# Optimization experiments

Measured on AMD Instinct MI355X. Metric: run time of the kernel, lower is better.

## Reference

```python
import jax, jax.numpy as jnp
import numpy as np

N_NODES = 100000
N_USER = 50000
D_IN = 100     # n_units[0]
F_OUT = 16     # n_units[1]
N_HEAD = 3     # n_heads[0]
N_TYPES = 3    # nb_nodes
N_EDGES = 1600000
D2 = 128


def setup_inputs() -> dict:
    key = jax.random.key(0)
    ks = jax.random.split(key, 9)
    h = jax.random.normal(ks[0], (N_NODES, D_IN), dtype=jnp.float32)
    edge_index = jax.random.randint(ks[1], (N_TYPES, 2, N_EDGES), 0, N_NODES, dtype=jnp.int64)
    # per-type GAT params (torch Linear stored transposed: (in, out))
    W = jax.random.normal(ks[2], (N_TYPES, D_IN, N_HEAD * F_OUT), dtype=jnp.float32) * 0.1
    b = jax.random.normal(ks[3], (N_TYPES, N_HEAD * F_OUT), dtype=jnp.float32) * 0.1
    a_src = jax.random.normal(ks[4], (N_TYPES, N_HEAD, F_OUT), dtype=jnp.float32) * 0.1
    a_trg = jax.random.normal(ks[5], (N_TYPES, N_HEAD, F_OUT), dtype=jnp.float32) * 0.1
    # additive attention params
    w1 = jax.random.normal(ks[6], (D_IN, D2), dtype=jnp.float32) * 0.1
    w2 = jax.random.normal(ks[7], (F_OUT, D2), dtype=jnp.float32) * 0.1
    m = jax.random.normal(ks[8], (D2, 1), dtype=jnp.float32) * 0.1
    return {"h": h, "W": W, "b": b, "a_src": a_src, "a_trg": a_trg,
            "w1": w1, "w2": w2, "m": m, "edge_index": edge_index}


def _sparse_gat(h, src, trg, W, b, a_src, a_trg):
    """Single SparseMultiHeadGraphAttention layer followed by head-mean."""
    N = h.shape[0]
    h_prime = (h @ W + b).reshape(N, N_HEAD, F_OUT)  # (N, H, F)
    hs = h_prime[src]                                # (E', H, F) edge gather
    # NOTE: faithful to source — both scores use the src-gathered features
    e = (hs * a_src).sum(-1) + (hs * a_trg).sum(-1)  # (E', H)
    e = jax.nn.leaky_relu(e, negative_slope=0.2)
    e = e - e.max()                                  # global max (as in source)
    exp_e = jnp.exp(e)
    denom = jax.ops.segment_sum(exp_e, trg, num_segments=N)      # (N, H)
    alpha = exp_e / (denom[trg] + 1e-10)                          # (E', H)
    out = jax.ops.segment_sum(hs * alpha[..., None], trg, num_segments=N)  # (N, H, F)
    return out.mean(axis=1)  # == permute(1,0,2).mean(dim=0)


def reference(h, W, b, a_src, a_trg, w1, w2, m, edge_index):
    N = h.shape[0]
    loop = jnp.arange(N, dtype=edge_index.dtype)
    embs = []
    for t in range(N_TYPES):  # small fixed set of relation types
        src = jnp.concatenate([edge_index[t, 0], loop])  # add self-loops
        trg = jnp.concatenate([edge_index[t, 1], loop])
        x = _sparse_gat(h, src, trg, W[t], b[t], a_src[t], a_trg[t])
        embs.append(x[:N_USER])
    type_aware = jnp.stack(embs, axis=1)  # (Nu, |Rs|, F)
    feat = h[:N_USER]                     # (Nu, D)
    # additive attention over types
    q = jnp.tanh((feat @ w1)[:, None, :] + type_aware @ w2)  # (Nu, |Rs|, D2)
    scores = (q @ m)[..., 0]                                  # (Nu, |Rs|)
    beta = jax.nn.softmax(scores, axis=1)
    fusion = jnp.einsum('nr,nrf->nf', beta, type_aware)[:, None, :]  # (Nu,1,F)
    return jnp.concatenate([fusion, type_aware], axis=1)  # (Nu, |Rs|+1, F)
```

## Files before the change

kernel.cpp:

```cpp
#include <hip/hip_runtime.h>
#include <hip/hip_bf16.h>

#define N_NODES 100000
#define N_USER  50000
#define D_IN    100
#define F_OUT   16
#define N_HEAD  3
#define N_TYPES 3
#define N_EDGES 1600000
#define D2      128
#define N_SEG   (N_TYPES * N_USER)
#define KP      136
#define CAP     64
#define CAPH    32
#define NBLK    ((N_NODES + 63) / 64)
#define NPAIR   (N_TYPES * N_EDGES / 2)
#define NBIN    256
#define SEGB    586
#define NBLKA   782
#define PAIRS_A 3072
#define CAPPB   40

typedef __hip_bfloat16 bf16;
typedef __attribute__((ext_vector_type(8))) short bf16x8;
typedef __attribute__((ext_vector_type(4))) float f32x4;
static __device__ __forceinline__ float b2f(bf16 x) { return __bfloat162float(x); }

#define OFF_CVT   64
#define OFF_CW    (OFF_CVT)
#define OFF_CB    (OFF_CW + 14400)
#define OFF_CAS   (OFF_CB + 144)
#define OFF_CAT   (OFF_CAS + 144)
#define OFF_CW1   (OFF_CAT + 144)
#define OFF_CW2   (OFF_CW1 + 12800)
#define OFF_CM    (OFF_CW2 + 2048)
#define CVT_TOTAL 29808
#define OFF_WT    29888
#define OFF_REC   49472
#define OFF_BUCKET OFF_REC
#define OFF_CPB   (OFF_REC + 9600000)
#define OFF_CA    (OFF_CPB + 240000)
#define OFF_CB2   (OFF_CA + 151000)
#define OFF_ELIST (OFF_CB2 + 151000)
#define OFF_TA    (OFF_ELIST + 9600000)
#define OFF_FW1   (OFF_TA + 2400000)

__global__ void k_detect(const unsigned* __restrict__ hraw,
                         const unsigned* __restrict__ eiraw,
                         int* __restrict__ flags) {
    __shared__ int sane, nz;
    if (threadIdx.x == 0) { sane = 0; nz = 0; }
    __syncthreads();
    int cnt = 0; unsigned o = 0;
    for (int i = threadIdx.x; i < 1024; i += 256) {
        unsigned w = hraw[i];
        unsigned e = (w >> 23) & 0xFF;
        if (e >= 64 && e <= 200) cnt++;
        o |= eiraw[2 * i + 1];
    }
    atomicAdd(&sane, cnt);
    atomicOr(&nz, (int)(o != 0));
    __syncthreads();
    if (threadIdx.x == 0) {
        flags[0] = (sane > 512) ? 1 : 0;
        flags[1] = nz ? 0 : 1;
    }
}

#define NBLK_CVT 117
#define NBLK_WT  153
__global__ __launch_bounds__(256) void k_prep(
        const void* __restrict__ W, const void* __restrict__ b,
        const void* __restrict__ as_, const void* __restrict__ at_,
        const void* __restrict__ w1, const void* __restrict__ w2,
        const void* __restrict__ m, const int* __restrict__ flags,
        float* __restrict__ cvt, ushort* __restrict__ wt) {
    if (blockIdx.x < NBLK_CVT) {
        int i = blockIdx.x * 256 + threadIdx.x;
        if (i >= CVT_TOTAL) return;
        const void* src; int off;
        if      (i < 14400)                 { src = W;   off = i; }
        else if (i < 14400+144)             { src = b;   off = i - 14400; }
        else if (i < 14400+288)             { src = as_; off = i - 14544; }
        else if (i < 14400+432)             { src = at_; off = i - 14688; }
        else if (i < 14400+432+12800)       { src = w1;  off = i - 14832; }
        else if (i < 14400+432+12800+2048)  { src = w2;  off = i - 27632; }
        else                                { src = m;   off = i - 29680; }
        cvt[i] = flags[0] ? ((const float*)src)[off] : b2f(((const bf16*)src)[off]);
    } else {
        int i = (blockIdx.x - NBLK_CVT) * 256 + threadIdx.x;
        if (i >= 6 * 48 * KP) return;
        int g = i / (48 * KP);
        int r = i - g * (48 * KP);
        int n = r / KP, k = r % KP;
        ushort v = 0;
        if (k < D_IN) {
            if (g < 3) {
                size_t src = ((size_t)g * D_IN + k) * 48 + n;
                if (flags[0]) { bf16 x = __float2bfloat16(((const float*)W)[src]); v = *(ushort*)&x; }
                else          { v = ((const ushort*)W)[src]; }
            } else {
                int c = (g - 3) * 48 + n;
                if (c < D2) {
                    size_t src = (size_t)k * D2 + c;
                    if (flags[0]) { bf16 x = __float2bfloat16(((const float*)w1)[src]); v = *(ushort*)&x; }
                    else          { v = ((const ushort*)w1)[src]; }
                }
            }
        }
        wt[i] = v;
    }
}

static __device__ __forceinline__ int2 load_ei2(const void* ei, int f64, size_t pairPos) {
    if (f64) {
        int4 v = ((const int4*)ei)[pairPos];
        int2 r; r.x = v.x; r.y = v.z; return r;
    }
    return ((const int2*)ei)[pairPos];
}

__global__ __launch_bounds__(256) void k_part(const void* __restrict__ ei,
                                              const int* __restrict__ flags,
                                              unsigned* __restrict__ bucket,
                                              unsigned* __restrict__ cpb) {
    __shared__ int bc[NBIN];
    const int f64ei = flags[1];
    const int NE2 = N_EDGES >> 1;
    const int tid = threadIdx.x;
    const int blk = blockIdx.x;
    if (tid < NBIN) bc[tid] = 0;
    __syncthreads();
    const int pair0 = blk * PAIRS_A;
    int npair = NPAIR - pair0; if (npair > PAIRS_A) npair = PAIRS_A;
#pragma unroll
    for (int q = 0; q < PAIRS_A / 256; ++q) {
        int pp = q * 256 + tid;
        int ok = (pp < npair);
        int pg = pair0 + (ok ? pp : 0);
        int t  = (pg >= 2 * NE2) ? 2 : ((pg >= NE2) ? 1 : 0);
        int ep = pg - t * NE2;
        int2 tg = load_ei2(ei, f64ei, (size_t)(t * 2 + 1) * NE2 + ep);
        int2 sr = load_ei2(ei, f64ei, (size_t)(t * 2) * NE2 + ep);
        if (ok && (unsigned)tg.x < N_USER) {
            int seg = t * N_USER + tg.x;
            int bin = seg & 255;
            int pos = atomicAdd(&bc[bin], 1);
            if (pos < CAPPB)
                bucket[((size_t)bin * NBLKA + blk) * CAPPB + pos] =
                    ((unsigned)(seg >> 8) << 17) | (unsigned)sr.x;
        }
        if (ok && (unsigned)tg.y < N_USER) {
            int seg = t * N_USER + tg.y;
            int bin = seg & 255;
            int pos = atomicAdd(&bc[bin], 1);
            if (pos < CAPPB)
                bucket[((size_t)bin * NBLKA + blk) * CAPPB + pos] =
                    ((unsigned)(seg >> 8) << 17) | (unsigned)sr.y;
        }
    }
    __syncthreads();
    if (tid < NBIN) cpb[(size_t)tid * NBLKA + blk] = (unsigned)bc[tid];
}

__global__ __launch_bounds__(256) void k_place(const unsigned* __restrict__ bucket,
                                               const unsigned* __restrict__ cpb,
                                               int* __restrict__ elist,
                                               unsigned* __restrict__ cA,
                                               unsigned* __restrict__ cBv) {
    __shared__ int sc[SEGB];
    const int bin = blockIdx.x >> 1;
    const int h   = blockIdx.x & 1;
    const int tid = threadIdx.x;
    for (int i = tid; i < SEGB; i += 256) sc[i] = 0;
    __syncthreads();
    const int rn = NBLKA / 2;
    for (int j = tid; j < rn; j += 256) {
        int r = 2 * j + h;
        int c = (int)cpb[(size_t)bin * NBLKA + r];
        if (c > CAPPB) c = CAPPB;
        size_t base = ((size_t)bin * NBLKA + r) * CAPPB;
        for (int i4 = 0; i4 < (c + 3) >> 2; ++i4) {
            uint4 wv = *(const uint4*)&bucket[base + 4 * i4];
#pragma unroll
            for (int k = 0; k < 4; ++k) {
                int idx = 4 * i4 + k;
                if (idx < c) {
                    unsigned e = (k == 0) ? wv.x : (k == 1) ? wv.y : (k == 2) ? wv.z : wv.w;
                    int sl  = (int)(e >> 17);
                    int src = (int)(e & 0x1FFFFu);
                    int pos = atomicAdd(&sc[sl], 1);
                    if (pos < CAPH) {
                        int seg = (sl << 8) + bin;
                        int t = seg / N_USER;
                        elist[(size_t)seg * CAP + (h << 5) + pos] =
                            (t * N_NODES + src) << 7;
                    }
                }
            }
        }
    }
    __syncthreads();
    for (int s = tid; s < SEGB; s += 256) {
        int seg = (s << 8) + bin;
        if (seg < N_SEG) {
            int cc = sc[s]; if (cc > CAPH) cc = CAPH;
            if (h) cBv[seg] = (unsigned)cc; else cA[seg] = (unsigned)cc;
        }
    }
}

__global__ __launch_bounds__(256) void k_hp_pack(const void* __restrict__ h,
                                                 const ushort* __restrict__ wtg,
                                                 const float* __restrict__ cb,
                                                 const float* __restrict__ cas,
                                                 const float* __restrict__ cat,
                                                 const int* __restrict__ flags,
                                                 float* __restrict__ fw1G,
                                                 float* __restrict__ rec) {
    __shared__ alignas(16) ushort hs[64][KP];
    __shared__ alignas(16) unsigned img[64 * 36];
    const int tid = threadIdx.x;
    const int node0 = blockIdx.x * 64;
    const int f32in = flags[0];
    for (int i = tid; i < 64 * KP; i += 256) {
        int r = i / KP, c = i % KP;
        int n = node0 + r;
        ushort v = 0;
        if (c < D_IN && n < N_NODES) {
            if (f32in) {
                bf16 t16 = __float2bfloat16(((const float*)h)[(size_t)n * D_IN + c]);
                v = *(ushort*)&t16;
            } else {
                v = ((const ushort*)h)[(size_t)n * D_IN + c];
            }
        }
        hs[r][c] = v;
    }
    __syncthreads();
    const int lane = tid & 63;
    const int w    = tid >> 6;
    const int m    = lane & 15;
    const int quad = lane >> 4;
    ushort* img16 = (ushort*)img;
    const int elig = (node0 < N_USER);
    const int nphase = elig ? 6 : 3;
    for (int p = 0; p < nphase; ++p) {
        const ushort* wp = wtg + (size_t)p * 48 * KP;
        f32x4 acc0 = {0.f, 0.f, 0.f, 0.f}, acc1 = acc0, acc2 = acc0;
#pragma unroll
        for (int ks = 0; ks < 4; ++ks) {
            int ko = ks * 32 + quad * 8;
            bf16x8 a  = *(const bf16x8*)&hs[w * 16 + m][ko];
            bf16x8 b0 = *(const bf16x8*)&wp[(0 * 16 + m) * KP + ko];
            bf16x8 b1 = *(const bf16x8*)&wp[(1 * 16 + m) * KP + ko];
            bf16x8 b2 = *(const bf16x8*)&wp[(2 * 16 + m) * KP + ko];
            acc0 = __builtin_amdgcn_mfma_f32_16x16x32_bf16(a, b0, acc0, 0, 0, 0);
            acc1 = __builtin_amdgcn_mfma_f32_16x16x32_bf16(a, b1, acc1, 0, 0, 0);
            acc2 = __builtin_amdgcn_mfma_f32_16x16x32_bf16(a, b2, acc2, 0, 0, 0);
        }
        if (p < 3) {
            const int t = p;
            float hpv[3][4], sred[3][4];
#pragma unroll
            for (int nt = 0; nt < 3; ++nt) {
                int col = nt * 16 + m;
                float bv = cb[t * 48 + col];
                float av = cas[t * 48 + col] + cat[t * 48 + col];
                f32x4 a4 = (nt == 0) ? acc0 : (nt == 1) ? acc1 : acc2;
#pragma unroll
                for (int r = 0; r < 4; ++r) {
                    hpv[nt][r] = a4[r] + bv;
                    sred[nt][r] = hpv[nt][r] * av;
                }
            }
#pragma unroll
            for (int d = 1; d < 16; d <<= 1) {
#pragma unroll
                for (int nt = 0; nt < 3; ++nt)
#pragma unroll
                    for (int r = 0; r < 4; ++r)
                        sred[nt][r] += __shfl_xor(sred[nt][r], d);
            }
            float pk[3][4];
#pragma unroll
            for (int nt = 0; nt < 3; ++nt)
#pragma unroll
                for (int r = 0; r < 4; ++r) {
                    float s = sred[nt][r];
                    s = (s > 0.f) ? s : 0.2f * s;
                    pk[nt][r] = __expf(s);
                }
            __syncthreads();
#pragma unroll
            for (int nt = 0; nt < 3; ++nt) {
                int col = nt * 16 + m;
#pragma unroll
                for (int r = 0; r < 4; ++r) {
                    int row = w * 16 + quad * 4 + r;
                    bf16 gb = __float2bfloat16(pk[nt][r] * hpv[nt][r]);
                    img16[row * 72 + col] = *(ushort*)&gb;
                }
            }
            if (m < 8) {
#pragma unroll
                for (int r = 0; r < 4; ++r) {
                    int row = w * 16 + quad * 4 + r;
                    img[row * 36 + 24 + m] = (m < 3) ? __float_as_uint(pk[m][r]) : 0u;
                }
            }
            __syncthreads();
            {
                int r = tid >> 2, q = tid & 3;
                int n = node0 + r;
                if (n < N_NODES) {
                    const uint4* s = (const uint4*)&img[r * 36 + q * 8];
                    uint4 x0 = s[0], x1 = s[1];
                    uint4* d = (uint4*)((unsigned*)rec + ((size_t)t * N_NODES + n) * 32 + q * 8);
                    d[0] = x0; d[1] = x1;
                }
            }
        } else {
            const int chunk = p - 3;
#pragma unroll
            for (int nt = 0; nt < 3; ++nt) {
                int col = chunk * 48 + nt * 16 + m;
                if (col < D2) {
                    f32x4 a4 = (nt == 0) ? acc0 : (nt == 1) ? acc1 : acc2;
#pragma unroll
                    for (int r = 0; r < 4; ++r) {
                        int row = w * 16 + quad * 4 + r;
                        int v = node0 + row;
                        if (v < N_USER) fw1G[(size_t)v * D2 + col] = a4[r];
                    }
                }
            }
        }
    }
}

__global__ __launch_bounds__(256) void k_gather(const float* __restrict__ rec,
                                                const int* __restrict__ elist,
                                                const unsigned* __restrict__ cA,
                                                const unsigned* __restrict__ cBv,
                                                float* __restrict__ ta) {
    int wid = (blockIdx.x * 256 + threadIdx.x) >> 6;
    if (wid >= N_SEG) return;
    int lane = threadIdx.x & 63;
    int t = wid / N_USER, v = wid - t * N_USER;
    int h = lane >> 5, l = lane & 31;
    const char* recc = (const char*)rec;
    const unsigned l4 = (unsigned)(l << 2);
    const bool isg = (l < 24);
    const int      s0m = isg ? 16 : 0;
    const unsigned m0  = isg ? 0xFFFF0000u : 0xFFFFFFFFu;
    const unsigned m1  = isg ? 0xFFFF0000u : 0u;
    int ev = elist[(size_t)wid * CAP + lane];
    int a = (int)cA[wid];
    int b = (int)cBv[wid];
    unsigned wself = 0u;
    if (h == 0)
        wself = *(const unsigned*)(recc + (((unsigned)(t * N_NODES + v)) << 7) + l4);
    float a0 = 0.f, a1 = 0.f;
    const int myn = h ? b : a;
    const int mx = a > b ? a : b;
    const int hbase = h << 5;
    for (int i0 = 0; i0 < mx; i0 += 12) {
        unsigned w[12];
#pragma unroll
        for (int q = 0; q < 12; ++q) {
            w[q] = 0u;
            int ee = i0 + q;
            int off = __shfl(ev, hbase + (ee & 31));
            if (ee < myn)
                w[q] = *(const unsigned*)(recc + (unsigned)off + l4);
        }
        __builtin_amdgcn_sched_barrier(0);
#pragma unroll
        for (int q = 0; q < 12; ++q) {
            a0 += __uint_as_float((w[q] << s0m) & m0);
            a1 += __uint_as_float(w[q] & m1);
        }
    }
    a0 += __uint_as_float((wself << s0m) & m0);
    a1 += __uint_as_float(wself & m1);
    a0 += __shfl_xor(a0, 32);
    a1 += __shfl_xor(a1, 32);
    int k = (l >> 3); if (k > 2) k = 2;
    float dk = __shfl(a0, 24 + k) + 1e-10f;
    float r0 = a0 / dk, r1 = a1 / dk;
    float sf0 = r0 + __shfl(r0, (l & 7) + 8) + __shfl(r0, (l & 7) + 16);
    float sf1 = r1 + __shfl(r1, (l & 7) + 8) + __shfl(r1, (l & 7) + 16);
    if (lane < 8) {
        float2 o;
        o.x = sf0 * (1.f / 3.f);
        o.y = sf1 * (1.f / 3.f);
        *(float2*)&ta[(size_t)v * 48 + t * 16 + 2 * lane] = o;
    }
}

__global__ __launch_bounds__(256) void k_fuse(const float* __restrict__ fw1G,
                                              const float* __restrict__ cw2,
                                              const float* __restrict__ cm,
                                              const float* __restrict__ ta,
                                              const int* __restrict__ flags,
                                              void* __restrict__ out) {
    __shared__ float w2s[F_OUT * D2];
    __shared__ float ms[D2];
    __shared__ float tas[64][49];
    __shared__ float psum[64][12];
    __shared__ float fus[64][16];
    const int tid = threadIdx.x;
    const int v0 = blockIdx.x * 64;
    const int f32in = flags[0];
    for (int i = tid; i < F_OUT * D2; i += 256) w2s[i] = cw2[i];
    if (tid < D2) ms[tid] = cm[tid];
    {
        int r = tid >> 2, c4 = (tid & 3) * 12;
        int v = v0 + r;
        for (int j = 0; j < 12; ++j)
            tas[r][c4 + j] = (v < N_USER) ? ta[(size_t)v * 48 + c4 + j] : 0.f;
    }
    __syncthreads();
    const int u  = tid & 63;
    const int og = tid >> 6;
    const int v  = v0 + u;
    float tr[48];
#pragma unroll
    for (int x = 0; x < 48; ++x) tr[x] = tas[u][x];
    float acc[2][16];
#pragma unroll
    for (int ph = 0; ph < 2; ++ph) {
        if (v < N_USER) {
            const float4* fr = (const float4*)&fw1G[(size_t)v * D2 + ph * 64 + og * 16];
#pragma unroll
            for (int q = 0; q < 4; ++q) {
                float4 x = fr[q];
                acc[ph][q * 4 + 0] = x.x;
                acc[ph][q * 4 + 1] = x.y;
                acc[ph][q * 4 + 2] = x.z;
                acc[ph][q * 4 + 3] = x.w;
            }
        } else {
#pragma unroll
            for (int j = 0; j < 16; ++j) acc[ph][j] = 0.f;
        }
    }
    float part[3] = {0.f, 0.f, 0.f};
#pragma unroll
    for (int ph = 0; ph < 2; ++ph) {
#pragma unroll
        for (int j = 0; j < 16; ++j) {
            int c = ph * 64 + og * 16 + j;
            float fv = acc[ph][j];
            float mv = ms[c];
#pragma unroll
            for (int t = 0; t < 3; ++t) {
                float z = fv;
#pragma unroll
                for (int f = 0; f < 16; ++f)
                    z += tr[t * 16 + f] * w2s[f * D2 + c];
                float q = 1.f - 2.f / (__expf(2.f * z) + 1.f);
                part[t] += q * mv;
            }
        }
    }
    psum[u][og * 3 + 0] = part[0];
    psum[u][og * 3 + 1] = part[1];
    psum[u][og * 3 + 2] = part[2];
    __syncthreads();
    if (tid < 64) {
        float sc[3];
#pragma unroll
        for (int t = 0; t < 3; ++t)
            sc[t] = psum[tid][t] + psum[tid][3 + t] + psum[tid][6 + t] + psum[tid][9 + t];
        float mx = fmaxf(sc[0], fmaxf(sc[1], sc[2]));
        float e0 = __expf(sc[0] - mx), e1 = __expf(sc[1] - mx), e2 = __expf(sc[2] - mx);
        float inv = 1.f / (e0 + e1 + e2);
#pragma unroll
        for (int f = 0; f < 16; ++f)
            fus[tid][f] = (e0 * tas[tid][f] + e1 * tas[tid][16 + f] + e2 * tas[tid][32 + f]) * inv;
    }
    __syncthreads();
    for (int kq = 0; kq < 16; ++kq) {
        int lin = kq * 256 + tid;
        int r = lin >> 6, c = lin & 63;
        int vv = v0 + r;
        if (vv < N_USER) {
            float val = (c < 16) ? fus[r][c] : tas[r][c - 16];
            size_t oidx = (size_t)vv * 64 + c;
            if (f32in) ((float*)out)[oidx] = val;
            else       ((bf16*)out)[oidx]  = __float2bfloat16(val);
        }
    }
}

extern "C" void kernel_launch(void* const* d_in, const int* in_sizes, int n_in,
                              void* d_out, int out_size, void* d_ws, size_t ws_size,
                              hipStream_t stream) {
    float* ws = (float*)d_ws;
    int*   flags = (int*)ws;
    float* cvt   = ws + OFF_CVT;
    float* cb    = ws + OFF_CB;
    float* cas   = ws + OFF_CAS;
    float* cat   = ws + OFF_CAT;
    float* cw2   = ws + OFF_CW2;
    float* cm    = ws + OFF_CM;
    ushort* wt   = (ushort*)(ws + OFF_WT);
    float* rec   = ws + OFF_REC;
    unsigned* bucket = (unsigned*)(ws + OFF_BUCKET);
    unsigned* cpb    = (unsigned*)(ws + OFF_CPB);
    unsigned* cA     = (unsigned*)(ws + OFF_CA);
    unsigned* cBv    = (unsigned*)(ws + OFF_CB2);
    int*   elist = (int*)(ws + OFF_ELIST);
    float* ta    = ws + OFF_TA;
    float* fw1   = ws + OFF_FW1;

    k_detect<<<1, 256, 0, stream>>>((const unsigned*)d_in[0], (const unsigned*)d_in[8], flags);
    k_prep<<<NBLK_CVT + NBLK_WT, 256, 0, stream>>>(
        d_in[1], d_in[2], d_in[3], d_in[4], d_in[5], d_in[6], d_in[7], flags, cvt, wt);

    k_part<<<NBLKA, 256, 0, stream>>>(d_in[8], flags, bucket, cpb);
    k_place<<<NBIN * 2, 256, 0, stream>>>(bucket, cpb, elist, cA, cBv);

    k_hp_pack<<<NBLK, 256, 0, stream>>>(
        d_in[0], wt, cb, cas, cat, flags, fw1, rec);

    k_gather<<<(N_SEG * 64 + 255) / 256, 256, 0, stream>>>(rec, elist, cA, cBv, ta);

    k_fuse<<<(N_USER + 63) / 64, 256, 0, stream>>>(fw1, cw2, cm, ta, flags, d_out);
}
```

Before: 377.8 us.

## Merge independent prep/partition and place/pack kernels into combined launches

```diff
diff --git a/kernel.cpp b/kernel.cpp
--- a/kernel.cpp
+++ b/kernel.cpp
@@ -20,6 +20,8 @@
 #define NBLKA   782
 #define PAIRS_A 3072
 #define CAPPB   40
+#define NPREPB  270
+#define NPLACE  512
 
 typedef __hip_bfloat16 bf16;
 typedef __attribute__((ext_vector_type(8))) short bf16x8;
@@ -37,7 +39,7 @@
 #define CVT_TOTAL 29808
 #define OFF_WT    29888
 #define OFF_REC   49472
-#define OFF_BUCKET OFF_REC
+#define OFF_BUCKET (OFF_REC + 9600000 + 240000 + 302000 + 9600000 + 2400000 + 6406144)
 #define OFF_CPB   (OFF_REC + 9600000)
 #define OFF_CA    (OFF_CPB + 240000)
 #define OFF_CB2   (OFF_CA + 151000)
@@ -67,16 +69,27 @@
     }
 }
 
+static __device__ __forceinline__ int2 load_ei2(const void* ei, int f64, size_t pairPos) {
+    if (f64) {
+        int4 v = ((const int4*)ei)[pairPos];
+        int2 r; r.x = v.x; r.y = v.z; return r;
+    }
+    return ((const int2*)ei)[pairPos];
+}
+
 #define NBLK_CVT 117
-#define NBLK_WT  153
-__global__ __launch_bounds__(256) void k_prep(
+__global__ __launch_bounds__(256) void k_prep_part(
         const void* __restrict__ W, const void* __restrict__ b,
         const void* __restrict__ as_, const void* __restrict__ at_,
         const void* __restrict__ w1, const void* __restrict__ w2,
-        const void* __restrict__ m, const int* __restrict__ flags,
-        float* __restrict__ cvt, ushort* __restrict__ wt) {
+        const void* __restrict__ m, const void* __restrict__ ei,
+        const int* __restrict__ flags,
+        float* __restrict__ cvt, ushort* __restrict__ wt,
+        unsigned* __restrict__ bucket, unsigned* __restrict__ cpb) {
+    __shared__ int bc[NBIN];
+    const int tid = threadIdx.x;
     if (blockIdx.x < NBLK_CVT) {
-        int i = blockIdx.x * 256 + threadIdx.x;
+        int i = blockIdx.x * 256 + tid;
         if (i >= CVT_TOTAL) return;
         const void* src; int off;
         if      (i < 14400)                 { src = W;   off = i; }
@@ -87,8 +100,8 @@
         else if (i < 14400+432+12800+2048)  { src = w2;  off = i - 27632; }
         else                                { src = m;   off = i - 29680; }
         cvt[i] = flags[0] ? ((const float*)src)[off] : b2f(((const bf16*)src)[off]);
-    } else {
-        int i = (blockIdx.x - NBLK_CVT) * 256 + threadIdx.x;
+    } else if (blockIdx.x < NPREPB) {
+        int i = (blockIdx.x - NBLK_CVT) * 256 + tid;
         if (i >= 6 * 48 * KP) return;
         int g = i / (48 * KP);
         int r = i - g * (48 * KP);
@@ -109,229 +122,225 @@
             }
         }
         wt[i] = v;
-    }
-}
-
-static __device__ __forceinline__ int2 load_ei2(const void* ei, int f64, size_t pairPos) {
-    if (f64) {
-        int4 v = ((const int4*)ei)[pairPos];
-        int2 r; r.x = v.x; r.y = v.z; return r;
-    }
-    return ((const int2*)ei)[pairPos];
-}
-
-__global__ __launch_bounds__(256) void k_part(const void* __restrict__ ei,
-                                              const int* __restrict__ flags,
-                                              unsigned* __restrict__ bucket,
-                                              unsigned* __restrict__ cpb) {
-    __shared__ int bc[NBIN];
-    const int f64ei = flags[1];
-    const int NE2 = N_EDGES >> 1;
+    } else {
+        const int blk = blockIdx.x - NPREPB;
+        const int f64ei = flags[1];
+        const int NE2 = N_EDGES >> 1;
+        if (tid < NBIN) bc[tid] = 0;
+        __syncthreads();
+        const int pair0 = blk * PAIRS_A;
+        int npair = NPAIR - pair0; if (npair > PAIRS_A) npair = PAIRS_A;
+#pragma unroll
+        for (int q = 0; q < PAIRS_A / 256; ++q) {
+            int pp = q * 256 + tid;
+            int ok = (pp < npair);
+            int pg = pair0 + (ok ? pp : 0);
+            int t  = (pg >= 2 * NE2) ? 2 : ((pg >= NE2) ? 1 : 0);
+            int ep = pg - t * NE2;
+            int2 tg = load_ei2(ei, f64ei, (size_t)(t * 2 + 1) * NE2 + ep);
+            int2 sr = load_ei2(ei, f64ei, (size_t)(t * 2) * NE2 + ep);
+            if (ok && (unsigned)tg.x < N_USER) {
+                int seg = t * N_USER + tg.x;
+                int bin = seg & 255;
+                int pos = atomicAdd(&bc[bin], 1);
+                if (pos < CAPPB)
+                    bucket[((size_t)bin * NBLKA + blk) * CAPPB + pos] =
+                        ((unsigned)(seg >> 8) << 17) | (unsigned)sr.x;
+            }
+            if (ok && (unsigned)tg.y < N_USER) {
+                int seg = t * N_USER + tg.y;
+                int bin = seg & 255;
+                int pos = atomicAdd(&bc[bin], 1);
+                if (pos < CAPPB)
+                    bucket[((size_t)bin * NBLKA + blk) * CAPPB + pos] =
+                        ((unsigned)(seg >> 8) << 17) | (unsigned)sr.y;
+            }
+        }
+        __syncthreads();
+        if (tid < NBIN) cpb[(size_t)tid * NBLKA + blk] = (unsigned)bc[tid];
+    }
+}
+
+__global__ __launch_bounds__(256) void k_place_pack(
+        const unsigned* __restrict__ bucket, const unsigned* __restrict__ cpb,
+        int* __restrict__ elist, unsigned* __restrict__ cA,
+        unsigned* __restrict__ cBv,
+        const void* __restrict__ h, const ushort* __restrict__ wtg,
+        const float* __restrict__ cb, const float* __restrict__ cas,
+        const float* __restrict__ cat, const int* __restrict__ flags,
+        float* __restrict__ fw1G, float* __restrict__ rec) {
+    __shared__ alignas(16) unsigned char smem[26624];
     const int tid = threadIdx.x;
-    const int blk = blockIdx.x;
-    if (tid < NBIN) bc[tid] = 0;
-    __syncthreads();
-    const int pair0 = blk * PAIRS_A;
-    int npair = NPAIR - pair0; if (npair > PAIRS_A) npair = PAIRS_A;
-#pragma unroll
-    for (int q = 0; q < PAIRS_A / 256; ++q) {
-        int pp = q * 256 + tid;
-        int ok = (pp < npair);
-        int pg = pair0 + (ok ? pp : 0);
-        int t  = (pg >= 2 * NE2) ? 2 : ((pg >= NE2) ? 1 : 0);
-        int ep = pg - t * NE2;
-        int2 tg = load_ei2(ei, f64ei, (size_t)(t * 2 + 1) * NE2 + ep);
-        int2 sr = load_ei2(ei, f64ei, (size_t)(t * 2) * NE2 + ep);
-        if (ok && (unsigned)tg.x < N_USER) {
-            int seg = t * N_USER + tg.x;
-            int bin = seg & 255;
-            int pos = atomicAdd(&bc[bin], 1);
-            if (pos < CAPPB)
-                bucket[((size_t)bin * NBLKA + blk) * CAPPB + pos] =
-                    ((unsigned)(seg >> 8) << 17) | (unsigned)sr.x;
-        }
-        if (ok && (unsigned)tg.y < N_USER) {
-            int seg = t * N_USER + tg.y;
-            int bin = seg & 255;
-            int pos = atomicAdd(&bc[bin], 1);
-            if (pos < CAPPB)
-                bucket[((size_t)bin * NBLKA + blk) * CAPPB + pos] =
-                    ((unsigned)(seg >> 8) << 17) | (unsigned)sr.y;
-        }
-    }
-    __syncthreads();
-    if (tid < NBIN) cpb[(size_t)tid * NBLKA + blk] = (unsigned)bc[tid];
-}
-
-__global__ __launch_bounds__(256) void k_place(const unsigned* __restrict__ bucket,
-                                               const unsigned* __restrict__ cpb,
-                                               int* __restrict__ elist,
-                                               unsigned* __restrict__ cA,
-                                               unsigned* __restrict__ cBv) {
-    __shared__ int sc[SEGB];
-    const int bin = blockIdx.x >> 1;
-    const int h   = blockIdx.x & 1;
-    const int tid = threadIdx.x;
-    for (int i = tid; i < SEGB; i += 256) sc[i] = 0;
-    __syncthreads();
-    const int rn = NBLKA / 2;
-    for (int j = tid; j < rn; j += 256) {
-        int r = 2 * j + h;
-        int c = (int)cpb[(size_t)bin * NBLKA + r];
-        if (c > CAPPB) c = CAPPB;
-        size_t base = ((size_t)bin * NBLKA + r) * CAPPB;
-        for (int i4 = 0; i4 < (c + 3) >> 2; ++i4) {
-            uint4 wv = *(const uint4*)&bucket[base + 4 * i4];
-#pragma unroll
-            for (int k = 0; k < 4; ++k) {
-                int idx = 4 * i4 + k;
-                if (idx < c) {
-                    unsigned e = (k == 0) ? wv.x : (k == 1) ? wv.y : (k == 2) ? wv.z : wv.w;
-                    int sl  = (int)(e >> 17);
-                    int src = (int)(e & 0x1FFFFu);
-                    int pos = atomicAdd(&sc[sl], 1);
-                    if (pos < CAPH) {
-                        int seg = (sl << 8) + bin;
-                        int t = seg / N_USER;
-                        elist[(size_t)seg * CAP + (h << 5) + pos] =
-                            (t * N_NODES + src) << 7;
-                    }
-                }
-            }
-        }
-    }
-    __syncthreads();
-    for (int s = tid; s < SEGB; s += 256) {
-        int seg = (s << 8) + bin;
-        if (seg < N_SEG) {
-            int cc = sc[s]; if (cc > CAPH) cc = CAPH;
-            if (h) cBv[seg] = (unsigned)cc; else cA[seg] = (unsigned)cc;
-        }
-    }
-}
-
-__global__ __launch_bounds__(256) void k_hp_pack(const void* __restrict__ h,
-                                                 const ushort* __restrict__ wtg,
-                                                 const float* __restrict__ cb,
-                                                 const float* __restrict__ cas,
-                                                 const float* __restrict__ cat,
-                                                 const int* __restrict__ flags,
-                                                 float* __restrict__ fw1G,
-                                                 float* __restrict__ rec) {
-    __shared__ alignas(16) ushort hs[64][KP];
-    __shared__ alignas(16) unsigned img[64 * 36];
-    const int tid = threadIdx.x;
-    const int node0 = blockIdx.x * 64;
-    const int f32in = flags[0];
-    for (int i = tid; i < 64 * KP; i += 256) {
-        int r = i / KP, c = i % KP;
-        int n = node0 + r;
-        ushort v = 0;
-        if (c < D_IN && n < N_NODES) {
-            if (f32in) {
-                bf16 t16 = __float2bfloat16(((const float*)h)[(size_t)n * D_IN + c]);
-                v = *(ushort*)&t16;
-            } else {
-                v = ((const ushort*)h)[(size_t)n * D_IN + c];
-            }
-        }
-        hs[r][c] = v;
-    }
-    __syncthreads();
-    const int lane = tid & 63;
-    const int w    = tid >> 6;
-    const int m    = lane & 15;
-    const int quad = lane >> 4;
-    ushort* img16 = (ushort*)img;
-    const int elig = (node0 < N_USER);
-    const int nphase = elig ? 6 : 3;
-    for (int p = 0; p < nphase; ++p) {
-        const ushort* wp = wtg + (size_t)p * 48 * KP;
-        f32x4 acc0 = {0.f, 0.f, 0.f, 0.f}, acc1 = acc0, acc2 = acc0;
-#pragma unroll
-        for (int ks = 0; ks < 4; ++ks) {
-            int ko = ks * 32 + quad * 8;
-            bf16x8 a  = *(const bf16x8*)&hs[w * 16 + m][ko];
-            bf16x8 b0 = *(const bf16x8*)&wp[(0 * 16 + m) * KP + ko];
-            bf16x8 b1 = *(const bf16x8*)&wp[(1 * 16 + m) * KP + ko];
-            bf16x8 b2 = *(const bf16x8*)&wp[(2 * 16 + m) * KP + ko];
-            acc0 = __builtin_amdgcn_mfma_f32_16x16x32_bf16(a, b0, acc0, 0, 0, 0);
-            acc1 = __builtin_amdgcn_mfma_f32_16x16x32_bf16(a, b1, acc1, 0, 0, 0);
-            acc2 = __builtin_amdgcn_mfma_f32_16x16x32_bf16(a, b2, acc2, 0, 0, 0);
-        }
-        if (p < 3) {
-            const int t = p;
-            float hpv[3][4], sred[3][4];
-#pragma unroll
-            for (int nt = 0; nt < 3; ++nt) {
-                int col = nt * 16 + m;
-                float bv = cb[t * 48 + col];
-                float av = cas[t * 48 + col] + cat[t * 48 + col];
-                f32x4 a4 = (nt == 0) ? acc0 : (nt == 1) ? acc1 : acc2;
-#pragma unroll
-                for (int r = 0; r < 4; ++r) {
-                    hpv[nt][r] = a4[r] + bv;
-                    sred[nt][r] = hpv[nt][r] * av;
-                }
-            }
-#pragma unroll
-            for (int d = 1; d < 16; d <<= 1) {
+    if (blockIdx.x < NPLACE) {
+        int* sc = (int*)smem;
+        const int bin = blockIdx.x >> 1;
+        const int hf  = blockIdx.x & 1;
+        for (int i = tid; i < SEGB; i += 256) sc[i] = 0;
+        __syncthreads();
+        const int rn = NBLKA / 2;
+        for (int j = tid; j < rn; j += 256) {
+            int r = 2 * j + hf;
+            int c = (int)cpb[(size_t)bin * NBLKA + r];
+            if (c > CAPPB) c = CAPPB;
+            size_t base = ((size_t)bin * NBLKA + r) * CAPPB;
+            for (int i4 = 0; i4 < (c + 3) >> 2; ++i4) {
+                uint4 wv = *(const uint4*)&bucket[base + 4 * i4];
+#pragma unroll
+                for (int k = 0; k < 4; ++k) {
+                    int idx = 4 * i4 + k;
+                    if (idx < c) {
+                        unsigned e = (k == 0) ? wv.x : (k == 1) ? wv.y : (k == 2) ? wv.z : wv.w;
+                        int sl  = (int)(e >> 17);
+                        int src = (int)(e & 0x1FFFFu);
+                        int pos = atomicAdd(&sc[sl], 1);
+                        if (pos < CAPH) {
+                            int seg = (sl << 8) + bin;
+                            int t = seg / N_USER;
+                            elist[(size_t)seg * CAP + (hf << 5) + pos] =
+                                (t * N_NODES + src) << 7;
+                        }
+                    }
+                }
+            }
+        }
+        __syncthreads();
+        for (int s = tid; s < SEGB; s += 256) {
+            int seg = (s << 8) + bin;
+            if (seg < N_SEG) {
+                int cc = sc[s]; if (cc > CAPH) cc = CAPH;
+                if (hf) cBv[seg] = (unsigned)cc; else cA[seg] = (unsigned)cc;
+            }
+        }
+    } else {
+        ushort (*hs)[KP] = reinterpret_cast<ushort(*)[KP]>(smem);
+        unsigned* img = (unsigned*)(smem + 17408);
+        const int node0 = (blockIdx.x - NPLACE) * 64;
+        const int f32in = flags[0];
+        if (f32in) {
+            const float* hfp = (const float*)h;
+            for (int i = tid; i < 64 * 25; i += 256) {
+                int r = i / 25, ch = i - r * 25;
+                int n = node0 + r;
+                ushort4 s4 = make_ushort4(0, 0, 0, 0);
+                if (n < N_NODES) {
+                    float4 x = *(const float4*)&hfp[(size_t)n * D_IN + ch * 4];
+                    bf16 b0 = __float2bfloat16(x.x), b1 = __float2bfloat16(x.y);
+                    bf16 b2 = __float2bfloat16(x.z), b3 = __float2bfloat16(x.w);
+                    s4 = make_ushort4(*(ushort*)&b0, *(ushort*)&b1, *(ushort*)&b2, *(ushort*)&b3);
+                }
+                *(ushort4*)&hs[r][ch * 4] = s4;
+            }
+        } else {
+            const ushort* hu = (const ushort*)h;
+            for (int i = tid; i < 64 * 25; i += 256) {
+                int r = i / 25, ch = i - r * 25;
+                int n = node0 + r;
+                uint2 v = make_uint2(0, 0);
+                if (n < N_NODES)
+                    v = *(const uint2*)&hu[(size_t)n * D_IN + ch * 4];
+                *(uint2*)&hs[r][ch * 4] = v;
+            }
+        }
+        for (int i = tid; i < 64 * 9; i += 256) {
+            int r = i / 9, ch = i - r * 9;
+            *(uint2*)&hs[r][100 + ch * 4] = make_uint2(0, 0);
+        }
+        __syncthreads();
+        const int lane = tid & 63;
+        const int w    = tid >> 6;
+        const int m    = lane & 15;
+        const int quad = lane >> 4;
+        ushort* img16 = (ushort*)img;
+        const int elig = (node0 < N_USER);
+        const int nphase = elig ? 6 : 3;
+        for (int p = 0; p < nphase; ++p) {
+            const ushort* wp = wtg + (size_t)p * 48 * KP;
+            f32x4 acc0 = {0.f, 0.f, 0.f, 0.f}, acc1 = acc0, acc2 = acc0;
+#pragma unroll
+            for (int ks = 0; ks < 4; ++ks) {
+                int ko = ks * 32 + quad * 8;
+                bf16x8 a  = *(const bf16x8*)&hs[w * 16 + m][ko];
+                bf16x8 b0 = *(const bf16x8*)&wp[(0 * 16 + m) * KP + ko];
+                bf16x8 b1 = *(const bf16x8*)&wp[(1 * 16 + m) * KP + ko];
+                bf16x8 b2 = *(const bf16x8*)&wp[(2 * 16 + m) * KP + ko];
+                acc0 = __builtin_amdgcn_mfma_f32_16x16x32_bf16(a, b0, acc0, 0, 0, 0);
+                acc1 = __builtin_amdgcn_mfma_f32_16x16x32_bf16(a, b1, acc1, 0, 0, 0);
+                acc2 = __builtin_amdgcn_mfma_f32_16x16x32_bf16(a, b2, acc2, 0, 0, 0);
+            }
+            if (p < 3) {
+                const int t = p;
+                float hpv[3][4], sred[3][4];
+#pragma unroll
+                for (int nt = 0; nt < 3; ++nt) {
+                    int col = nt * 16 + m;
+                    float bv = cb[t * 48 + col];
+                    float av = cas[t * 48 + col] + cat[t * 48 + col];
+                    f32x4 a4 = (nt == 0) ? acc0 : (nt == 1) ? acc1 : acc2;
+#pragma unroll
+                    for (int r = 0; r < 4; ++r) {
+                        hpv[nt][r] = a4[r] + bv;
+                        sred[nt][r] = hpv[nt][r] * av;
+                    }
+                }
+#pragma unroll
+                for (int d = 1; d < 16; d <<= 1) {
+#pragma unroll
+                    for (int nt = 0; nt < 3; ++nt)
+#pragma unroll
+                        for (int r = 0; r < 4; ++r)
+                            sred[nt][r] += __shfl_xor(sred[nt][r], d);
+                }
+                float pk[3][4];
 #pragma unroll
                 for (int nt = 0; nt < 3; ++nt)
 #pragma unroll
-                    for (int r = 0; r < 4; ++r)
-                        sred[nt][r] += __shfl_xor(sred[nt][r], d);
-            }
-            float pk[3][4];
-#pragma unroll
-            for (int nt = 0; nt < 3; ++nt)
-#pragma unroll
-                for (int r = 0; r < 4; ++r) {
-                    float s = sred[nt][r];
-                    s = (s > 0.f) ? s : 0.2f * s;
-                    pk[nt][r] = __expf(s);
-                }
-            __syncthreads();
-#pragma unroll
-            for (int nt = 0; nt < 3; ++nt) {
-                int col = nt * 16 + m;
-#pragma unroll
-                for (int r = 0; r < 4; ++r) {
-                    int row = w * 16 + quad * 4 + r;
-                    bf16 gb = __float2bfloat16(pk[nt][r] * hpv[nt][r]);
-                    img16[row * 72 + col] = *(ushort*)&gb;
-                }
-            }
-            if (m < 8) {
-#pragma unroll
-                for (int r = 0; r < 4; ++r) {
-                    int row = w * 16 + quad * 4 + r;
-                    img[row * 36 + 24 + m] = (m < 3) ? __float_as_uint(pk[m][r]) : 0u;
-                }
-            }
-            __syncthreads();
-            {
-                int r = tid >> 2, q = tid & 3;
-                int n = node0 + r;
-                if (n < N_NODES) {
-                    const uint4* s = (const uint4*)&img[r * 36 + q * 8];
-                    uint4 x0 = s[0], x1 = s[1];
-                    uint4* d = (uint4*)((unsigned*)rec + ((size_t)t * N_NODES + n) * 32 + q * 8);
-                    d[0] = x0; d[1] = x1;
-                }
-            }
-        } else {
-            const int chunk = p - 3;
-#pragma unroll
-            for (int nt = 0; nt < 3; ++nt) {
-                int col = chunk * 48 + nt * 16 + m;
-                if (col < D2) {
-                    f32x4 a4 = (nt == 0) ? acc0 : (nt == 1) ? acc1 : acc2;
+                    for (int r = 0; r < 4; ++r) {
+                        float s = sred[nt][r];
+                        s = (s > 0.f) ? s : 0.2f * s;
+                        pk[nt][r] = __expf(s);
+                    }
+                __syncthreads();
+#pragma unroll
+                for (int nt = 0; nt < 3; ++nt) {
+                    int col = nt * 16 + m;
 #pragma unroll
                     for (int r = 0; r < 4; ++r) {
                         int row = w * 16 + quad * 4 + r;
-                        int v = node0 + row;
-                        if (v < N_USER) fw1G[(size_t)v * D2 + col] = a4[r];
+                        bf16 gb = __float2bfloat16(pk[nt][r] * hpv[nt][r]);
+                        img16[row * 72 + col] = *(ushort*)&gb;
+                    }
+                }
+                if (m < 8) {
+#pragma unroll
+                    for (int r = 0; r < 4; ++r) {
+                        int row = w * 16 + quad * 4 + r;
+                        img[row * 36 + 24 + m] = (m < 3) ? __float_as_uint(pk[m][r]) : 0u;
+                    }
+                }
+                __syncthreads();
+                {
+                    int r = tid >> 2, q = tid & 3;
+                    int n = node0 + r;
+                    if (n < N_NODES) {
+                        const uint4* s = (const uint4*)&img[r * 36 + q * 8];
+                        uint4 x0 = s[0], x1 = s[1];
+                        uint4* d = (uint4*)((unsigned*)rec + ((size_t)t * N_NODES + n) * 32 + q * 8);
+                        d[0] = x0; d[1] = x1;
+                    }
+                }
+            } else {
+                const int chunk = p - 3;
+#pragma unroll
+                for (int nt = 0; nt < 3; ++nt) {
+                    int col = chunk * 48 + nt * 16 + m;
+                    if (col < D2) {
+                        f32x4 a4 = (nt == 0) ? acc0 : (nt == 1) ? acc1 : acc2;
+#pragma unroll
+                        for (int r = 0; r < 4; ++r) {
+                            int row = w * 16 + quad * 4 + r;
+                            int v = node0 + row;
+                            if (v < N_USER) fw1G[(size_t)v * D2 + col] = a4[r];
+                        }
                     }
                 }
             }
@@ -517,13 +526,13 @@
     float* fw1   = ws + OFF_FW1;
 
     k_detect<<<1, 256, 0, stream>>>((const unsigned*)d_in[0], (const unsigned*)d_in[8], flags);
-    k_prep<<<NBLK_CVT + NBLK_WT, 256, 0, stream>>>(
-        d_in[1], d_in[2], d_in[3], d_in[4], d_in[5], d_in[6], d_in[7], flags, cvt, wt);
-
-    k_part<<<NBLKA, 256, 0, stream>>>(d_in[8], flags, bucket, cpb);
-    k_place<<<NBIN * 2, 256, 0, stream>>>(bucket, cpb, elist, cA, cBv);
-
-    k_hp_pack<<<NBLK, 256, 0, stream>>>(
+
+    k_prep_part<<<NPREPB + NBLKA, 256, 0, stream>>>(
+        d_in[1], d_in[2], d_in[3], d_in[4], d_in[5], d_in[6], d_in[7], d_in[8],
+        flags, cvt, wt, bucket, cpb);
+
+    k_place_pack<<<NPLACE + NBLK, 256, 0, stream>>>(
+        bucket, cpb, elist, cA, cBv,
         d_in[0], wt, cb, cas, cat, flags, fw1, rec);
 
     k_gather<<<(N_SEG * 64 + 255) / 256, 256, 0, stream>>>(rec, elist, cA, cBv, ta);
```

Result: faster. 347.9 us (median of 2 runs) (-7.9%).
